# Kernel tuning notes

Measured on AMD Instinct MI355X. Metric: run time of the kernel, lower is better.

## Reference

```python
import jax, jax.numpy as jnp
import numpy as np

B, N, D, H = 4, 512, 64, 1
IN = 2 * D + 1  # edge_mlp input dim (edge_dim = 0)


def setup_inputs() -> dict:
    key = jax.random.key(0)
    ks = jax.random.split(key, 16)
    s = 0.05
    f32 = jnp.float32
    return dict(
        h=jax.random.normal(ks[0], (B, N, D), f32),
        x=jax.random.normal(ks[1], (B, N, 3), f32),
        rij=jax.random.normal(ks[2], (B, N, N, 3), f32),
        dij=jax.random.uniform(ks[3], (B, N, N), f32),
        mask=jnp.ones((B, N), f32),
        # edge_mlp: Linear(IN,H) SiLU Linear(H,H) SiLU Linear(H,1)
        eW1=(jax.random.normal(ks[4], (IN, H), f32) * s), eb1=jnp.zeros((H,), f32),
        eW2=(jax.random.normal(ks[5], (H, H), f32) * s), eb2=jnp.zeros((H,), f32),
        eW3=(jax.random.normal(ks[6], (H, 1), f32) * s), eb3=jnp.zeros((1,), f32),
        # phi_x: Linear(H,H) SiLU Linear(H,1), applied to m_ij[...,None] (last dim 1 == H)
        pW1=(jax.random.normal(ks[7], (H, H), f32) * s), pb1=jnp.zeros((H,), f32),
        pW2=(jax.random.normal(ks[8], (H, 1), f32) * s), pb2=jnp.zeros((1,), f32),
        # msg_to_node: Linear(H,H) SiLU Linear(H,D)
        nW1=(jax.random.normal(ks[9], (H, H), f32) * s), nb1=jnp.zeros((H,), f32),
        nW2=(jax.random.normal(ks[10], (H, D), f32) * s), nb2=jnp.zeros((D,), f32),
        # GRUCell(D, D)
        Wih=(jax.random.normal(ks[11], (3 * D, D), f32) * s), bih=jnp.zeros((3 * D,), f32),
        Whh=(jax.random.normal(ks[12], (3 * D, D), f32) * s), bhh=jnp.zeros((3 * D,), f32),
    )


def reference(h, x, rij, dij, mask,
              eW1, eb1, eW2, eb2, eW3, eb3,
              pW1, pb1, pW2, pb2,
              nW1, nb1, nW2, nb2,
              Wih, bih, Whh, bhh):
    Bs, Ns, Ds = h.shape
    hi = jnp.broadcast_to(h[:, :, None, :], (Bs, Ns, Ns, Ds))
    hj = jnp.broadcast_to(h[:, None, :, :], (Bs, Ns, Ns, Ds))
    edge_in = jnp.concatenate([hi, hj, dij[..., None]], axis=-1)  # (B,N,N,2D+1)
    m = jax.nn.silu(edge_in @ eW1 + eb1)
    m = jax.nn.silu(m @ eW2 + eb2)
    m_ij = (m @ eW3 + eb3)[..., 0]  # (B,N,N)
    pair_mask = mask[:, :, None] * mask[:, None, :]
    m_ij = m_ij * pair_mask
    mu = m_ij[..., None]  # (B,N,N,1)
    phi = jax.nn.silu(mu @ pW1 + pb1) @ pW2 + pb2  # (B,N,N,1)
    x_new = x + (rij * phi).sum(axis=2)  # (B,N,3)
    m_vec = jax.nn.silu(mu @ nW1 + nb1) @ nW2 + nb2  # (B,N,N,D)
    m_node = m_vec.sum(axis=2)  # (B,N,D)
    # GRUCell: input = m_node, hidden = h
    gi = m_node @ Wih.T + bih
    gh = h @ Whh.T + bhh
    i_r, i_z, i_n = jnp.split(gi, 3, axis=-1)
    h_r, h_z, h_n = jnp.split(gh, 3, axis=-1)
    r = jax.nn.sigmoid(i_r + h_r)
    z = jax.nn.sigmoid(i_z + h_z)
    n = jnp.tanh(i_n + r * h_n)
    h_new = (1.0 - z) * n + z * h
    h_new = h_new * mask[..., None]
    return (h_new, x_new)
```

## Files before the change

### kernel.cpp

```cpp
#include <hip/hip_runtime.h>
#include <hip/hip_bf16.h>


#define NB 512
#define DB 64
#define ROWS 2048
#define H_ELEMS (ROWS * DB)

__device__ __forceinline__ float silu(float x) { return x / (1.0f + __expf(-x)); }
__device__ __forceinline__ float sigmf(float x) { return 1.0f / (1.0f + __expf(-x)); }

__global__ __launch_bounds__(256) void egnn_pre(
    const float* __restrict__ h, const float* __restrict__ eW1,
    const float* __restrict__ nW2, const float* __restrict__ nb2,
    const float* __restrict__ Wih, const float* __restrict__ bih,
    float* __restrict__ A, float* __restrict__ C,
    float* __restrict__ U, float* __restrict__ V)
{
    int t = blockIdx.x * blockDim.x + threadIdx.x;
    if (t < ROWS) {
        const float* hr = h + (size_t)t * DB;
        float sa = 0.0f, sc = 0.0f;
        #pragma unroll 8
        for (int d = 0; d < DB; ++d) {
            float hv = hr[d];
            sa += hv * eW1[d];
            sc += hv * eW1[DB + d];
        }
        A[t] = sa; C[t] = sc;
    } else if (t < ROWS + 3 * DB) {
        int k = t - ROWS;
        const float* wr = Wih + (size_t)k * DB;
        float su = 0.0f, sv = 0.0f;
        #pragma unroll 8
        for (int d = 0; d < DB; ++d) {
            float w = wr[d];
            su += nW2[d] * w;
            sv += nb2[d] * w;
        }
        U[k] = su;
        V[k] = bih[k] + (float)NB * sv;
    }
}

__global__ __launch_bounds__(256) void egnn_main(
    const float* __restrict__ h, const float* __restrict__ x,
    const float* __restrict__ rij, const float* __restrict__ dij,
    const float* __restrict__ mask,
    const float* __restrict__ eW1, const float* __restrict__ eb1,
    const float* __restrict__ eW2, const float* __restrict__ eb2,
    const float* __restrict__ eW3, const float* __restrict__ eb3,
    const float* __restrict__ pW1, const float* __restrict__ pb1,
    const float* __restrict__ pW2, const float* __restrict__ pb2,
    const float* __restrict__ nW1, const float* __restrict__ nb1,
    const float* __restrict__ Whh, const float* __restrict__ bhh,
    const float* __restrict__ A, const float* __restrict__ C,
    const float* __restrict__ U, const float* __restrict__ V,
    float* __restrict__ out)
{
    const int row = blockIdx.x;
    const int b   = row >> 9;
    const int tid = threadIdx.x;

    const float wd  = eW1[2 * DB];
    const float b1  = eb1[0];
    const float w2  = eW2[0],  b2_ = eb2[0];
    const float w3  = eW3[0],  b3  = eb3[0];
    const float pw1 = pW1[0],  pbi = pb1[0];
    const float pw2 = pW2[0],  pbo = pb2[0];
    const float nw1 = nW1[0],  nbi = nb1[0];

    const float ai = A[row];
    const float mi = mask[row];
    const float* Cb = C + (b << 9);
    const float* maskb = mask + (b << 9);
    const float* dr = dij + (size_t)row * NB;
    const float* rr = rij + (size_t)row * NB * 3;

    float S = 0.0f, x0 = 0.0f, x1 = 0.0f, x2 = 0.0f;

    #pragma unroll 2
    for (int j = tid; j < NB; j += 256) {
        float cj = Cb[j];
        float dv = dr[j];
        float mj = maskb[j];
        float e1  = ai + cj + wd * dv + b1;
        float m1  = silu(e1);
        float m2  = silu(m1 * w2 + b2_);
        float mij = (m2 * w3 + b3) * (mi * mj);
        float phi = silu(mij * pw1 + pbi) * pw2 + pbo;
        float s   = silu(mij * nw1 + nbi);
        S += s;
        int base = j * 3;
        x0 += rr[base + 0] * phi;
        x1 += rr[base + 1] * phi;
        x2 += rr[base + 2] * phi;
    }

    #pragma unroll
    for (int off = 32; off > 0; off >>= 1) {
        S  += __shfl_down(S,  off, 64);
        x0 += __shfl_down(x0, off, 64);
        x1 += __shfl_down(x1, off, 64);
        x2 += __shfl_down(x2, off, 64);
    }
    __shared__ float red[4][4];
    __shared__ float fin[4];
    __shared__ float hrow[DB];
    const int wave = tid >> 6, lane = tid & 63;
    if (lane == 0) { red[wave][0] = S; red[wave][1] = x0; red[wave][2] = x1; red[wave][3] = x2; }
    if (tid < DB) hrow[tid] = h[(size_t)row * DB + tid];
    __syncthreads();
    if (tid < 4) fin[tid] = red[0][tid] + red[1][tid] + red[2][tid] + red[3][tid];
    __syncthreads();

    if (tid < DB) {
        const float Sf = fin[0];
        const int d = tid;
        const float* Wr = Whh + (size_t)d * DB;
        const float* Wz = Whh + (size_t)(DB + d) * DB;
        const float* Wn = Whh + (size_t)(2 * DB + d) * DB;
        float ghr = bhh[d];
        float ghz = bhh[DB + d];
        float ghn = bhh[2 * DB + d];
        #pragma unroll 8
        for (int k = 0; k < DB; ++k) {
            float hv = hrow[k];
            ghr += hv * Wr[k];
            ghz += hv * Wz[k];
            ghn += hv * Wn[k];
        }
        float gir = Sf * U[d]          + V[d];
        float giz = Sf * U[DB + d]     + V[DB + d];
        float gin = Sf * U[2 * DB + d] + V[2 * DB + d];
        float r = sigmf(gir + ghr);
        float z = sigmf(giz + ghz);
        float n = tanhf(gin + r * ghn);
        float hn = (1.0f - z) * n + z * hrow[d];
        hn *= mi;
        out[(size_t)row * DB + d] = hn;
    } else if (tid < DB + 3) {
        const int ci = tid - DB;
        float xv = x[row * 3 + ci] + fin[1 + ci];
        out[H_ELEMS + row * 3 + ci] = xv;
    }
}

extern "C" void kernel_launch(void* const* d_in, const int* in_sizes, int n_in,
                              void* d_out, int out_size, void* d_ws, size_t ws_size,
                              hipStream_t stream) {
    const float* h    = (const float*)d_in[0];
    const float* x    = (const float*)d_in[1];
    const float* rij  = (const float*)d_in[2];
    const float* dij  = (const float*)d_in[3];
    const float* mask = (const float*)d_in[4];
    const float* eW1  = (const float*)d_in[5];
    const float* eb1  = (const float*)d_in[6];
    const float* eW2  = (const float*)d_in[7];
    const float* eb2  = (const float*)d_in[8];
    const float* eW3  = (const float*)d_in[9];
    const float* eb3  = (const float*)d_in[10];
    const float* pW1  = (const float*)d_in[11];
    const float* pb1  = (const float*)d_in[12];
    const float* pW2  = (const float*)d_in[13];
    const float* pb2  = (const float*)d_in[14];
    const float* nW1  = (const float*)d_in[15];
    const float* nb1  = (const float*)d_in[16];
    const float* nW2  = (const float*)d_in[17];
    const float* nb2  = (const float*)d_in[18];
    const float* Wih  = (const float*)d_in[19];
    const float* bih  = (const float*)d_in[20];
    const float* Whh  = (const float*)d_in[21];
    const float* bhh  = (const float*)d_in[22];

    float* A = (float*)d_ws;
    float* C = A + ROWS;
    float* U = C + ROWS;
    float* V = U + 3 * DB;

    egnn_pre<<<(ROWS + 3 * DB + 255) / 256, 256, 0, stream>>>(
        h, eW1, nW2, nb2, Wih, bih, A, C, U, V);

    egnn_main<<<ROWS, 256, 0, stream>>>(
        h, x, rij, dij, mask,
        eW1, eb1, eW2, eb2, eW3, eb3,
        pW1, pb1, pW2, pb2, nW1, nb1,
        Whh, bhh, A, C, U, V,
        (float*)d_out);
}
```

Before: 123.9 us.

## Precompute GRU hidden gates in tiled pre-kernel and vectorize main-loop loads

Moves the h @ Whh^T GRU hidden-gate computation out of the per-row main kernel into the pre-kernel. There it runs as a shared-memory tiled matmul over 32-row blocks, with Whh transposed into LDS, and writes the results to a workspace buffer. The main kernel now reads the precomputed gates and loads C, dij, mask and rij as float2, processing two j per thread in a single pass. This removes the redundant per-block Whh reads, but the pre-kernel now runs only 65 blocks and adds a global round-trip for the gh values.

```diff
diff --git a/kernel.cpp b/kernel.cpp
--- a/kernel.cpp
+++ b/kernel.cpp
@@ -14,32 +14,86 @@
     const float* __restrict__ h, const float* __restrict__ eW1,
     const float* __restrict__ nW2, const float* __restrict__ nb2,
     const float* __restrict__ Wih, const float* __restrict__ bih,
+    const float* __restrict__ Whh, const float* __restrict__ bhh,
     float* __restrict__ A, float* __restrict__ C,
-    float* __restrict__ U, float* __restrict__ V)
+    float* __restrict__ U, float* __restrict__ V,
+    float* __restrict__ gh)
 {
-    int t = blockIdx.x * blockDim.x + threadIdx.x;
-    if (t < ROWS) {
-        const float* hr = h + (size_t)t * DB;
-        float sa = 0.0f, sc = 0.0f;
-        #pragma unroll 8
+    const int tid = threadIdx.x;
+    if (blockIdx.x < 64) {
+        __shared__ float hT[32 * 65];
+        __shared__ float WT[64 * 193];
+        const int rowbase = blockIdx.x * 32;
+
+        for (int idx = tid; idx < 32 * 64; idx += 256) {
+            int r = idx >> 6, d = idx & 63;
+            hT[r * 65 + d] = h[(size_t)rowbase * 64 + idx];
+        }
+        for (int idx = tid; idx < 192 * 64; idx += 256) {
+            int k = idx >> 6, d = idx & 63;
+            WT[d * 193 + k] = Whh[idx];
+        }
+        __syncthreads();
+
+        if (tid < 32) {
+            float sa = 0.0f, sc = 0.0f;
+            #pragma unroll 8
+            for (int d = 0; d < DB; ++d) {
+                float hv = hT[tid * 65 + d];
+                sa += hv * eW1[d];
+                sc += hv * eW1[DB + d];
+            }
+            A[rowbase + tid] = sa;
+            C[rowbase + tid] = sc;
+        }
+
+        const int lane = tid & 63, wv = tid >> 6;
+        float acc[3][8];
+        #pragma unroll
+        for (int kg = 0; kg < 3; ++kg)
+            #pragma unroll
+            for (int rg = 0; rg < 8; ++rg) acc[kg][rg] = 0.0f;
         for (int d = 0; d < DB; ++d) {
-            float hv = hr[d];
-            sa += hv * eW1[d];
-            sc += hv * eW1[DB + d];
-        }
-        A[t] = sa; C[t] = sc;
-    } else if (t < ROWS + 3 * DB) {
-        int k = t - ROWS;
-        const float* wr = Wih + (size_t)k * DB;
-        float su = 0.0f, sv = 0.0f;
-        #pragma unroll 8
-        for (int d = 0; d < DB; ++d) {
-            float w = wr[d];
-            su += nW2[d] * w;
-            sv += nb2[d] * w;
-        }
-        U[k] = su;
-        V[k] = bih[k] + (float)NB * sv;
+            float w0 = WT[d * 193 + lane];
+            float w1 = WT[d * 193 + 64 + lane];
+            float w2 = WT[d * 193 + 128 + lane];
+            #pragma unroll
+            for (int rg = 0; rg < 8; ++rg) {
+                float hv = hT[(wv + 4 * rg) * 65 + d];
+                acc[0][rg] += hv * w0;
+                acc[1][rg] += hv * w1;
+                acc[2][rg] += hv * w2;
+            }
+        }
+        #pragma unroll
+        for (int kg = 0; kg < 3; ++kg) {
+            float bb = bhh[kg * 64 + lane];
+            #pragma unroll
+            for (int rg = 0; rg < 8; ++rg) {
+                int r = wv + 4 * rg;
+                gh[(size_t)(rowbase + r) * 192 + kg * 64 + lane] = acc[kg][rg] + bb;
+            }
+        }
+    } else {
+        const int lane = tid & 63, wv = tid >> 6;
+        if (wv < 3) {
+            float nw  = nW2[lane];
+            float nbv = nb2[lane];
+            for (int kk = 0; kk < 64; ++kk) {
+                int k = wv * 64 + kk;
+                float w = Wih[(size_t)k * 64 + lane];
+                float su = nw * w, sv = nbv * w;
+                #pragma unroll
+                for (int off = 32; off > 0; off >>= 1) {
+                    su += __shfl_xor(su, off, 64);
+                    sv += __shfl_xor(sv, off, 64);
+                }
+                if (lane == kk) {
+                    U[k] = su;
+                    V[k] = bih[k] + (float)NB * sv;
+                }
+            }
+        }
     }
 }
 
@@ -53,9 +107,9 @@
     const float* __restrict__ pW1, const float* __restrict__ pb1,
     const float* __restrict__ pW2, const float* __restrict__ pb2,
     const float* __restrict__ nW1, const float* __restrict__ nb1,
-    const float* __restrict__ Whh, const float* __restrict__ bhh,
     const float* __restrict__ A, const float* __restrict__ C,
     const float* __restrict__ U, const float* __restrict__ V,
+    const float* __restrict__ gh,
     float* __restrict__ out)
 {
     const int row = blockIdx.x;
@@ -72,29 +126,42 @@
 
     const float ai = A[row];
     const float mi = mask[row];
-    const float* Cb = C + (b << 9);
-    const float* maskb = mask + (b << 9);
-    const float* dr = dij + (size_t)row * NB;
-    const float* rr = rij + (size_t)row * NB * 3;
+
+    const float2* c2  = (const float2*)(C + (b << 9));
+    const float2* mk2 = (const float2*)(mask + (b << 9));
+    const float2* dr2 = (const float2*)(dij + (size_t)row * NB);
+    const float2* rr2 = (const float2*)(rij + (size_t)row * NB * 3);
 
     float S = 0.0f, x0 = 0.0f, x1 = 0.0f, x2 = 0.0f;
 
-    #pragma unroll 2
-    for (int j = tid; j < NB; j += 256) {
-        float cj = Cb[j];
-        float dv = dr[j];
-        float mj = maskb[j];
-        float e1  = ai + cj + wd * dv + b1;
-        float m1  = silu(e1);
-        float m2  = silu(m1 * w2 + b2_);
-        float mij = (m2 * w3 + b3) * (mi * mj);
-        float phi = silu(mij * pw1 + pbi) * pw2 + pbo;
-        float s   = silu(mij * nw1 + nbi);
-        S += s;
-        int base = j * 3;
-        x0 += rr[base + 0] * phi;
-        x1 += rr[base + 1] * phi;
-        x2 += rr[base + 2] * phi;
+    {
+        float2 cj = c2[tid];
+        float2 dv = dr2[tid];
+        float2 mj = mk2[tid];
+        float2 ra = rr2[3 * tid];
+        float2 rb = rr2[3 * tid + 1];
+        float2 rc = rr2[3 * tid + 2];
+
+        {
+            float e1  = ai + cj.x + wd * dv.x + b1;
+            float m2  = silu(silu(e1) * w2 + b2_);
+            float mij = (m2 * w3 + b3) * (mi * mj.x);
+            float phi = silu(mij * pw1 + pbi) * pw2 + pbo;
+            S  += silu(mij * nw1 + nbi);
+            x0 += ra.x * phi;
+            x1 += ra.y * phi;
+            x2 += rb.x * phi;
+        }
+        {
+            float e1  = ai + cj.y + wd * dv.y + b1;
+            float m2  = silu(silu(e1) * w2 + b2_);
+            float mij = (m2 * w3 + b3) * (mi * mj.y);
+            float phi = silu(mij * pw1 + pbi) * pw2 + pbo;
+            S  += silu(mij * nw1 + nbi);
+            x0 += rb.y * phi;
+            x1 += rc.x * phi;
+            x2 += rc.y * phi;
+        }
     }
 
     #pragma unroll
@@ -106,43 +173,30 @@
     }
     __shared__ float red[4][4];
     __shared__ float fin[4];
-    __shared__ float hrow[DB];
     const int wave = tid >> 6, lane = tid & 63;
-    if (lane == 0) { red[wave][0] = S; red[wave][1] = x0; red[wave][2] = x1; red[wave][3] = x2; }
-    if (tid < DB) hrow[tid] = h[(size_t)row * DB + tid];
+    if (lane == 0) {
+        red[wave][0] = S; red[wave][1] = x0; red[wave][2] = x1; red[wave][3] = x2;
+    }
     __syncthreads();
     if (tid < 4) fin[tid] = red[0][tid] + red[1][tid] + red[2][tid] + red[3][tid];
     __syncthreads();
 
     if (tid < DB) {
+        const int d = tid;
         const float Sf = fin[0];
-        const int d = tid;
-        const float* Wr = Whh + (size_t)d * DB;
-        const float* Wz = Whh + (size_t)(DB + d) * DB;
-        const float* Wn = Whh + (size_t)(2 * DB + d) * DB;
-        float ghr = bhh[d];
-        float ghz = bhh[DB + d];
-        float ghn = bhh[2 * DB + d];
-        #pragma unroll 8
-        for (int k = 0; k < DB; ++k) {
-            float hv = hrow[k];
-            ghr += hv * Wr[k];
-            ghz += hv * Wz[k];
-            ghn += hv * Wn[k];
-        }
+        const float* ghr_ = gh + (size_t)row * 192;
+        float ghr = ghr_[d], ghz = ghr_[DB + d], ghn = ghr_[2 * DB + d];
         float gir = Sf * U[d]          + V[d];
         float giz = Sf * U[DB + d]     + V[DB + d];
         float gin = Sf * U[2 * DB + d] + V[2 * DB + d];
         float r = sigmf(gir + ghr);
         float z = sigmf(giz + ghz);
         float n = tanhf(gin + r * ghn);
-        float hn = (1.0f - z) * n + z * hrow[d];
-        hn *= mi;
-        out[(size_t)row * DB + d] = hn;
+        float hv = h[(size_t)row * DB + d];
+        out[(size_t)row * DB + d] = ((1.0f - z) * n + z * hv) * mi;
     } else if (tid < DB + 3) {
         const int ci = tid - DB;
-        float xv = x[row * 3 + ci] + fin[1 + ci];
-        out[H_ELEMS + row * 3 + ci] = xv;
+        out[H_ELEMS + row * 3 + ci] = x[row * 3 + ci] + fin[1 + ci];
     }
 }
 
@@ -173,18 +227,19 @@
     const float* Whh  = (const float*)d_in[21];
     const float* bhh  = (const float*)d_in[22];
 
-    float* A = (float*)d_ws;
-    float* C = A + ROWS;
-    float* U = C + ROWS;
-    float* V = U + 3 * DB;
-
-    egnn_pre<<<(ROWS + 3 * DB + 255) / 256, 256, 0, stream>>>(
-        h, eW1, nW2, nb2, Wih, bih, A, C, U, V);
+    float* A  = (float*)d_ws;
+    float* C  = A + ROWS;
+    float* U  = C + ROWS;
+    float* V  = U + 3 * DB;
+    float* gh = V + 3 * DB;
+
+    egnn_pre<<<65, 256, 0, stream>>>(
+        h, eW1, nW2, nb2, Wih, bih, Whh, bhh, A, C, U, V, gh);
 
     egnn_main<<<ROWS, 256, 0, stream>>>(
         h, x, rij, dij, mask,
         eW1, eb1, eW2, eb2, eW3, eb3,
         pW1, pb1, pW2, pb2, nW1, nb1,
-        Whh, bhh, A, C, U, V,
+        A, C, U, V, gh,
         (float*)d_out);
 }
```

After: 145.8 us. 1.18x slower.
